# Optimization experiments

Hardware: AMD Instinct MI355X
Metric: run time of the kernel (lower is better)

Reference implementation:

```python
import jax, jax.numpy as jnp
import numpy as np

B, T, D, H = 2, 1024, 1024, 16
DH = D // H
_PAIRS = [(0, 1), (0, 2), (0, 3), (1, 2), (1, 3), (2, 3)]
_J6 = jnp.array([[0, 0, 0, 0, 0, 1],
                 [0, 0, 0, 0, -1, 0],
                 [0, 0, 0, 1, 0, 0],
                 [0, 0, 1, 0, 0, 0],
                 [0, -1, 0, 0, 0, 0],
                 [1, 0, 0, 0, 0, 0]], dtype=jnp.float32)


def exterior(p1, p2):
    # Plucker coordinates of the line through 4-vectors p1, p2, L2-normalized.
    parts = [p1[..., i] * p2[..., j] - p1[..., j] * p2[..., i] for i, j in _PAIRS]
    L = jnp.stack(parts, axis=-1)  # (..., 6)
    n = jnp.maximum(jnp.linalg.norm(L, axis=-1, keepdims=True), 1e-12)
    return L / n


def setup_inputs() -> dict:
    key = jax.random.key(0)
    ks = jax.random.split(key, 10)
    s = 0.02
    return {
        "x": jax.random.normal(ks[0], (B, T, D), jnp.float32),
        "Wqkv": jax.random.normal(ks[1], (3 * D, D), jnp.float32) * s,
        "bqkv": jnp.zeros((3 * D,), jnp.float32),
        "W1w": jax.random.normal(ks[2], (4 * H, D), jnp.float32) * s,
        "W2w": jax.random.normal(ks[3], (4 * H, D), jnp.float32) * s,
        "W1r": jax.random.normal(ks[4], (4 * H, D), jnp.float32) * s,
        "W2r": jax.random.normal(ks[5], (4 * H, D), jnp.float32) * s,
        "bias_scale": jnp.full((H,), 0.1, jnp.float32),
        "Wout": jax.random.normal(ks[6], (D, D), jnp.float32) * s,
        "bout": jnp.zeros((D,), jnp.float32),
    }


def reference(x, Wqkv, bqkv, W1w, W2w, W1r, W2r, bias_scale, Wout, bout):
    Bb, Tt, Dd = x.shape
    scale = DH ** (-0.5)
    qkv = (x @ Wqkv.T + bqkv).reshape(Bb, Tt, 3, H, DH)
    q = jnp.transpose(qkv[:, :, 0], (0, 2, 1, 3))  # (B,H,T,dh)
    k = jnp.transpose(qkv[:, :, 1], (0, 2, 1, 3))
    v = jnp.transpose(qkv[:, :, 2], (0, 2, 1, 3))
    std_logits = jnp.einsum('bhtd,bhsd->bhts', q, k) * scale

    x_prev = jnp.concatenate([jnp.zeros((Bb, 1, Dd), x.dtype), x[:, :-1]], axis=1)
    w1 = (x_prev @ W1w.T).reshape(Bb, Tt, H, 4)
    w2 = (x @ W2w.T).reshape(Bb, Tt, H, 4)
    write_lines = exterior(w1, w2)  # (B,T,H,6)
    r1 = (x @ W1r.T).reshape(Bb, Tt, H, 4)
    r2 = (x @ W2r.T).reshape(Bb, Tt, H, 4)
    read_lines = exterior(r1, r2)  # (B,T,H,6)

    Jw = jnp.einsum('bthi,ij->bhtj', write_lines, _J6)  # (B,H,T,6)
    rd = jnp.transpose(read_lines, (0, 2, 1, 3))        # (B,H,T,6)

    outer = Jw[..., :, None] * Jw[..., None, :]          # (B,H,T,6,6)
    M_causal = jnp.cumsum(outer, axis=2)                 # running Gram state
    rd_M = jnp.einsum('bhti,bhtij->bhtj', rd, M_causal)  # (B,H,T,6)
    bias_raw = jnp.einsum('bhti,bhsi->bhts', rd_M, Jw)   # (B,H,T,T)
    bias = jnp.abs(bias_raw) * bias_scale.reshape(1, H, 1, 1)

    logits = std_logits + bias
    mask = jnp.triu(jnp.ones((Tt, Tt), bool), 1)
    logits = jnp.where(mask, -jnp.inf, logits)
    attn = jax.nn.softmax(logits, axis=-1)
    out = jnp.einsum('bhts,bhsd->bthd', attn, v).reshape(Bb, Tt, Dd)
    return out @ Wout.T + bout
```

## Files before the change

kernel.cpp:

```cpp
#include <hip/hip_runtime.h>
#include <math.h>

#define B_ 2
#define T_ 1024
#define D_ 1024
#define H_ 16
#define NA_ 3328

typedef __attribute__((ext_vector_type(8))) short bf16x8;
typedef __attribute__((ext_vector_type(4))) float f32x4;

__device__ inline unsigned short f2bf(float x) {
  return (unsigned short)((__float_as_uint(x) + 0x8000u) >> 16);
}
__device__ inline unsigned bfpack(float lo, float hi) {
  unsigned a = __float_as_uint(hi) + 0x8000u;
  unsigned b = __float_as_uint(lo) + 0x8000u;
  return __builtin_amdgcn_perm(a, b, 0x07060302);
}
__device__ inline void hl_split(float x, unsigned short& h, unsigned short& l) {
  unsigned short hh = f2bf(x);
  float hf = __uint_as_float(((unsigned)hh) << 16);
  l = f2bf(x - hf);
  h = hh;
}

#define G_PRO()                                                                \
  const int tid = threadIdx.x;                                                 \
  const int w = tid >> 6, lane = tid & 63;                                     \
  const int lr = lane & 15, g = lane >> 4;                                     \
  const int wm = (w >> 1) * 64, wn = (w & 1) * 64;                             \
  const int row = tid >> 1, half = tid & 1;

#define G_LOADA(d, s) {                                                        \
  d[0] = *(const float4*)(Ap + (s) * 32);                                      \
  d[1] = *(const float4*)(Ap + (s) * 32 + 4);                                  \
  d[2] = *(const float4*)(Ap + (s) * 32 + 8);                                  \
  d[3] = *(const float4*)(Ap + (s) * 32 + 12); }
#define G_LOADB(d, s) {                                                        \
  d[0] = *(const float4*)(Bp + (s) * 32);                                      \
  d[1] = *(const float4*)(Bp + (s) * 32 + 4);                                  \
  d[2] = *(const float4*)(Bp + (s) * 32 + 8);                                  \
  d[3] = *(const float4*)(Bp + (s) * 32 + 12); }
#define G_STORE(bi, a, b) {                                                    \
  unsigned char* SA_ = Smem + (bi) * 8192;                                     \
  uint4 lo = make_uint4(bfpack(a[0].x, a[0].y), bfpack(a[0].z, a[0].w),        \
                        bfpack(a[1].x, a[1].y), bfpack(a[1].z, a[1].w));       \
  uint4 hi = make_uint4(bfpack(a[2].x, a[2].y), bfpack(a[2].z, a[2].w),        \
                        bfpack(a[3].x, a[3].y), bfpack(a[3].z, a[3].w));       \
  *(uint4*)(SA_ + (half * 2 + 0) * 2048 + row * 16) = lo;                      \
  *(uint4*)(SA_ + (half * 2 + 1) * 2048 + row * 16) = hi;                      \
  unsigned char* SB_ = Smem + 16384 + (bi) * 8192;                             \
  lo = make_uint4(bfpack(b[0].x, b[0].y), bfpack(b[0].z, b[0].w),              \
                  bfpack(b[1].x, b[1].y), bfpack(b[1].z, b[1].w));             \
  hi = make_uint4(bfpack(b[2].x, b[2].y), bfpack(b[2].z, b[2].w),              \
                  bfpack(b[3].x, b[3].y), bfpack(b[3].z, b[3].w));             \
  *(uint4*)(SB_ + (half * 2 + 0) * 2048 + row * 16) = lo;                      \
  *(uint4*)(SB_ + (half * 2 + 1) * 2048 + row * 16) = hi; }
#define G_COMPUTE(bi) {                                                        \
  const unsigned char* SA_ = Smem + (bi) * 8192;                               \
  const unsigned char* SB_ = Smem + 16384 + (bi) * 8192;                       \
  bf16x8 af[4], bfr[4];                                                        \
  _Pragma("unroll") for (int i = 0; i < 4; ++i)                                \
    af[i] = *(const bf16x8*)(SA_ + g * 2048 + (wm + i * 16 + lr) * 16);        \
  _Pragma("unroll") for (int j = 0; j < 4; ++j)                                \
    bfr[j] = *(const bf16x8*)(SB_ + g * 2048 + (wn + j * 16 + lr) * 16);       \
  _Pragma("unroll") for (int i = 0; i < 4; ++i)                                \
  _Pragma("unroll") for (int j = 0; j < 4; ++j)                                \
    acc[i][j] = __builtin_amdgcn_mfma_f32_16x16x32_bf16(af[i], bfr[j],         \
                                                        acc[i][j], 0, 0, 0); }
#define G_MAIN()                                                               \
  f32x4 acc[4][4];                                                             \
  const f32x4 zf = {0.f, 0.f, 0.f, 0.f};                                       \
  _Pragma("unroll") for (int i = 0; i < 4; ++i)                                \
  _Pragma("unroll") for (int j = 0; j < 4; ++j) acc[i][j] = zf;                \
  float4 a0[4], b0[4], a1[4], b1[4];                                           \
  G_LOADA(a0, 0); G_LOADB(b0, 0);                                              \
  G_STORE(0, a0, b0);                                                          \
  G_LOADA(a1, 1); G_LOADB(b1, 1);                                              \
  __syncthreads();                                                             \
  _Pragma("unroll 1") for (int s = 0; s < 32; s += 2) {                        \
    G_COMPUTE(0);                                                              \
    G_STORE(1, a1, b1);                                                        \
    if (s + 2 < 32) { G_LOADA(a0, s + 2); G_LOADB(b0, s + 2); }                \
    __syncthreads();                                                           \
    G_COMPUTE(1);                                                              \
    if (s + 2 < 32) G_STORE(0, a0, b0);                                        \
    if (s + 3 < 32) { G_LOADA(a1, s + 3); G_LOADB(b1, s + 3); }                \
    __syncthreads();                                                           \
  }

__global__ __launch_bounds__(256) void gemm_qkv(
    const float* __restrict__ A, const float* __restrict__ Wqkv,
    const float* __restrict__ bqkv,
    const float* __restrict__ W1w, const float* __restrict__ W2w,
    const float* __restrict__ W1r, const float* __restrict__ W2r,
    float* __restrict__ C)
{
  __shared__ __align__(16) unsigned char Smem[32768];
  const int m0 = blockIdx.y * 128, n0 = blockIdx.x * 128;
  G_PRO();
  const float* Ap = A + (size_t)(m0 + row) * 1024 + half * 16;
  const float* Bp;
  {
    const int cg = n0 + row;
    if (cg < 3072) Bp = Wqkv + (size_t)cg * 1024;
    else {
      const int r2 = cg - 3072;
      const float* Wm = (r2 < 64) ? W1w : (r2 < 128) ? W2w : (r2 < 192) ? W1r : W2r;
      Bp = Wm + (size_t)(r2 & 63) * 1024;
    }
    Bp += half * 16;
  }
  G_MAIN();
#pragma unroll
  for (int i = 0; i < 4; ++i) {
    const int rbase = m0 + wm + i * 16 + 4 * g;
#pragma unroll
    for (int j = 0; j < 4; ++j) {
      const int col = n0 + wn + j * 16 + lr;
      const float bb = (col < 3072) ? bqkv[col] : 0.f;
#pragma unroll
      for (int r = 0; r < 4; ++r)
        C[(size_t)(rbase + r) * NA_ + col] = acc[i][j][r] + bb;
    }
  }
}

__global__ __launch_bounds__(256) void gemm_out(
    const float* __restrict__ A, const float* __restrict__ Bm,
    const float* __restrict__ bias, float* __restrict__ C)
{
  __shared__ __align__(16) unsigned char Smem[32768];
  const int m0 = blockIdx.y * 128, n0 = blockIdx.x * 128;
  G_PRO();
  const float* Ap = A + (size_t)(m0 + row) * 1024 + half * 16;
  const float* Bp = Bm + (size_t)(n0 + row) * 1024 + half * 16;
  G_MAIN();
#pragma unroll
  for (int i = 0; i < 4; ++i) {
    const int rbase = m0 + wm + i * 16 + 4 * g;
#pragma unroll
    for (int j = 0; j < 4; ++j) {
      const int col = n0 + wn + j * 16 + lr;
      const float bb = bias[col];
#pragma unroll
      for (int r = 0; r < 4; ++r)
        C[(size_t)(rbase + r) * 1024 + col] = acc[i][j][r] + bb;
    }
  }
}

__global__ __launch_bounds__(256) void exterior_kernel(
    const float* __restrict__ qkvp,
    float* __restrict__ Jw, float* __restrict__ rd,
    unsigned* __restrict__ Jwpk)
{
  const int i = blockIdx.x * 256 + threadIdx.x;
  const int h = i & 15;
  const int t = (i >> 4) & 1023;
  const int b = i >> 14;
  const size_t rowt = ((size_t)(b * T_) + t) * NA_;

  float4 p1w = make_float4(0.f, 0.f, 0.f, 0.f);
  if (t > 0) p1w = *(const float4*)(qkvp + rowt - NA_ + 3072 + h * 4);
  const float4 p2w = *(const float4*)(qkvp + rowt + 3136 + h * 4);
  const float4 p1r = *(const float4*)(qkvp + rowt + 3200 + h * 4);
  const float4 p2r = *(const float4*)(qkvp + rowt + 3264 + h * 4);

  const size_t base = ((size_t)(b * H_ + h) * T_ + t) * 6;
  {
    const float L0 = p1w.x * p2w.y - p1w.y * p2w.x;
    const float L1 = p1w.x * p2w.z - p1w.z * p2w.x;
    const float L2 = p1w.x * p2w.w - p1w.w * p2w.x;
    const float L3 = p1w.y * p2w.z - p1w.z * p2w.y;
    const float L4 = p1w.y * p2w.w - p1w.w * p2w.y;
    const float L5 = p1w.z * p2w.w - p1w.w * p2w.z;
    const float n = sqrtf(L0 * L0 + L1 * L1 + L2 * L2 + L3 * L3 + L4 * L4 + L5 * L5);
    const float inv = 1.f / fmaxf(n, 1e-12f);
    float jv[6] = {L5 * inv, -L4 * inv, L3 * inv, L2 * inv, -L1 * inv, L0 * inv};
#pragma unroll
    for (int k = 0; k < 6; ++k) Jw[base + k] = jv[k];
    unsigned short JH[6], JL[6];
#pragma unroll
    for (int k = 0; k < 6; ++k) hl_split(jv[k], JH[k], JL[k]);
    unsigned* jp = Jwpk + (((size_t)(b * H_ + h) * T_ + t) << 4);
    unsigned h01 = JH[0] | ((unsigned)JH[1] << 16);
    unsigned h23 = JH[2] | ((unsigned)JH[3] << 16);
    unsigned h45 = JH[4] | ((unsigned)JH[5] << 16);
    jp[0] = h01; jp[1] = h23; jp[2] = h45;
    jp[3] = JL[0] | ((unsigned)JL[1] << 16);
    jp[4] = JL[2] | ((unsigned)JL[3] << 16);
    jp[5] = JL[4] | ((unsigned)JL[5] << 16);
    jp[6] = h01; jp[7] = h23; jp[8] = h45;
#pragma unroll
    for (int k = 9; k < 16; ++k) jp[k] = 0;
  }
  {
    const float L0 = p1r.x * p2r.y - p1r.y * p2r.x;
    const float L1 = p1r.x * p2r.z - p1r.z * p2r.x;
    const float L2 = p1r.x * p2r.w - p1r.w * p2r.x;
    const float L3 = p1r.y * p2r.z - p1r.z * p2r.y;
    const float L4 = p1r.y * p2r.w - p1r.w * p2r.y;
    const float L5 = p1r.z * p2r.w - p1r.w * p2r.z;
    const float n = sqrtf(L0 * L0 + L1 * L1 + L2 * L2 + L3 * L3 + L4 * L4 + L5 * L5);
    const float inv = 1.f / fmaxf(n, 1e-12f);
    rd[base + 0] = L0 * inv;
    rd[base + 1] = L1 * inv;
    rd[base + 2] = L2 * inv;
    rd[base + 3] = L3 * inv;
    rd[base + 4] = L4 * inv;
    rd[base + 5] = L5 * inv;
  }
}

__global__ __launch_bounds__(256) void scan_kernel(
    const float* __restrict__ Jw, const float* __restrict__ rd,
    unsigned* __restrict__ rdMpk)
{
  __shared__ float sc[256][40];
  const int tid = threadIdx.x;
  const int bh = blockIdx.x;
  const float* Jb = Jw + (size_t)bh * T_ * 6;
  const float* Rb = rd + (size_t)bh * T_ * 6;
  const int t0 = tid * 4;

  float L[36], M[36];
#pragma unroll
  for (int i = 0; i < 36; ++i) L[i] = 0.f;
  for (int tt = 0; tt < 4; ++tt) {
    float j6[6];
#pragma unroll
    for (int i = 0; i < 6; ++i) j6[i] = Jb[(size_t)(t0 + tt) * 6 + i];
#pragma unroll
    for (int a = 0; a < 6; ++a)
#pragma unroll
      for (int c = 0; c < 6; ++c)
        L[a * 6 + c] = fmaf(j6[a], j6[c], L[a * 6 + c]);
  }
#pragma unroll
  for (int i = 0; i < 36; ++i) M[i] = L[i];
#pragma unroll
  for (int k = 0; k < 9; ++k)
    *(float4*)&sc[tid][k * 4] = make_float4(M[k*4], M[k*4+1], M[k*4+2], M[k*4+3]);
  __syncthreads();

  for (int off = 1; off < 256; off <<= 1) {
    float4 tmp[9];
    const bool act = (tid >= off);
    if (act) {
#pragma unroll
      for (int k = 0; k < 9; ++k) tmp[k] = *(const float4*)&sc[tid - off][k * 4];
    }
    __syncthreads();
    if (act) {
#pragma unroll
      for (int k = 0; k < 9; ++k) {
        M[k*4]   += tmp[k].x; M[k*4+1] += tmp[k].y;
        M[k*4+2] += tmp[k].z; M[k*4+3] += tmp[k].w;
      }
#pragma unroll
      for (int k = 0; k < 9; ++k)
        *(float4*)&sc[tid][k * 4] = make_float4(M[k*4], M[k*4+1], M[k*4+2], M[k*4+3]);
    }
    __syncthreads();
  }

  float Mp[36];
#pragma unroll
  for (int i = 0; i < 36; ++i) Mp[i] = M[i] - L[i];

  for (int tt = 0; tt < 4; ++tt) {
    const int t = t0 + tt;
    float j6[6], r6[6];
#pragma unroll
    for (int i = 0; i < 6; ++i) { j6[i] = Jb[(size_t)t * 6 + i]; r6[i] = Rb[(size_t)t * 6 + i]; }
#pragma unroll
    for (int a = 0; a < 6; ++a)
#pragma unroll
      for (int c = 0; c < 6; ++c)
        Mp[a * 6 + c] = fmaf(j6[a], j6[c], Mp[a * 6 + c]);
    float s6[6];
#pragma unroll
    for (int jj = 0; jj < 6; ++jj) {
      float s = 0.f;
#pragma unroll
      for (int a = 0; a < 6; ++a) s = fmaf(r6[a], Mp[a * 6 + jj], s);
      s6[jj] = s;
    }
    unsigned short hh[6], ll[6];
#pragma unroll
    for (int i = 0; i < 6; ++i) hl_split(s6[i], hh[i], ll[i]);
    unsigned* ob = rdMpk + (((size_t)bh * T_ + t) << 4);
    unsigned h01 = hh[0] | ((unsigned)hh[1] << 16);
    unsigned h23 = hh[2] | ((unsigned)hh[3] << 16);
    unsigned h45 = hh[4] | ((unsigned)hh[5] << 16);
    ob[0] = h01; ob[1] = h23; ob[2] = h45;
    ob[3] = h01; ob[4] = h23; ob[5] = h45;
    ob[6] = ll[0] | ((unsigned)ll[1] << 16);
    ob[7] = ll[2] | ((unsigned)ll[3] << 16);
    ob[8] = ll[4] | ((unsigned)ll[5] << 16);
#pragma unroll
    for (int i = 9; i < 16; ++i) ob[i] = 0;
  }
}

__global__ __launch_bounds__(256) void attn_mfma(
    const float* __restrict__ qkvp,
    const unsigned* __restrict__ Jwpk,
    const unsigned* __restrict__ rdMpk,
    const float* __restrict__ bias_scale,
    float* __restrict__ attnout)
{
  __shared__ __align__(16) unsigned char smem[40960];
  unsigned char* KT = smem;
  unsigned char* VT = smem + 16384;
  unsigned char* PB = smem + 32768;

  const int gid = blockIdx.x;
  const int bh = gid & 31;
  const int c = (gid < 256) ? (15 - (gid >> 5)) : ((gid - 256) >> 5);
  const int b = bh >> 4, h = bh & 15;
  const int tid = threadIdx.x;
  const int w = tid >> 6;
  const int lane = tid & 63;
  const int lr = lane & 15;
  const int g = lane >> 4;
  const int t0 = c * 64;
  const int nT = c + 1;

  const float* Rows = qkvp + (size_t)b * T_ * NA_ + h * 64;
  const size_t jb = (size_t)(b * H_ + h) * T_;

  bf16x8 qa[2];
  {
    const float* qp = Rows + (size_t)(t0 + w * 16 + lr) * NA_;
#pragma unroll
    for (int kb = 0; kb < 2; ++kb) {
      const float4 f0 = *(const float4*)(qp + kb * 32 + g * 8);
      const float4 f1 = *(const float4*)(qp + kb * 32 + g * 8 + 4);
      union { uint4 u; bf16x8 v; } qq;
      qq.u = make_uint4(bfpack(f0.x, f0.y), bfpack(f0.z, f0.w),
                        bfpack(f1.x, f1.y), bfpack(f1.z, f1.w));
      qa[kb] = qq.v;
    }
  }
  bf16x8 ra = *(const bf16x8*)(rdMpk + ((jb + t0 + w * 16 + lr) << 4) + g * 4);
  const float bsc = bias_scale[h];

  float m[4], lsum[4];
  f32x4 O[4];
  const f32x4 zf = {0.f, 0.f, 0.f, 0.f};
#pragma unroll
  for (int r = 0; r < 4; ++r) { m[r] = -1e30f; lsum[r] = 0.f; }
#pragma unroll
  for (int d = 0; d < 4; ++d) O[d] = zf;

  const int kr = tid >> 2, kc = tid & 3;
  const int sp = tid & 31, d8 = tid >> 5;

  float4 kA[4], vA0, vA1, vA2, vA3, kN[4], vN0, vN1, vN2, vN3;
  {
    const float* kp = Rows + (size_t)kr * NA_ + 1024 + kc * 16;
#pragma unroll
    for (int i = 0; i < 4; ++i) kA[i] = *(const float4*)(kp + i * 4);
    const float* vr = Rows + (size_t)(2 * sp) * NA_ + 2048 + d8 * 8;
    vA0 = *(const float4*)vr;         vA1 = *(const float4*)(vr + 4);
    vA2 = *(const float4*)(vr + NA_); vA3 = *(const float4*)(vr + NA_ + 4);
  }

  for (int ti = 0; ti < nT; ++ti) {
    const int s0 = ti * 64;
    const int buf = ti & 1;
    {
      unsigned char* kt = KT + buf * 8192;
      const float e[16] = {kA[0].x, kA[0].y, kA[0].z, kA[0].w,
                           kA[1].x, kA[1].y, kA[1].z, kA[1].w,
                           kA[2].x, kA[2].y, kA[2].z, kA[2].w,
                           kA[3].x, kA[3].y, kA[3].z, kA[3].w};
      const int swz = (kr & 7) << 4;
      uint4 w0, w1;
      w0.x = bfpack(e[0], e[1]);  w0.y = bfpack(e[2], e[3]);
      w0.z = bfpack(e[4], e[5]);  w0.w = bfpack(e[6], e[7]);
      w1.x = bfpack(e[8], e[9]);  w1.y = bfpack(e[10], e[11]);
      w1.z = bfpack(e[12], e[13]); w1.w = bfpack(e[14], e[15]);
      *(uint4*)(kt + kr * 128 + ((kc * 32) ^ swz))      = w0;
      *(uint4*)(kt + kr * 128 + ((kc * 32 + 16) ^ swz)) = w1;
    }
    {
      unsigned* vt = (unsigned*)(VT + buf * 8192);
      const float r0[8] = {vA0.x, vA0.y, vA0.z, vA0.w, vA1.x, vA1.y, vA1.z, vA1.w};
      const float r1[8] = {vA2.x, vA2.y, vA2.z, vA2.w, vA3.x, vA3.y, vA3.z, vA3.w};
#pragma unroll
      for (int i = 0; i < 8; ++i) {
        const int d = d8 * 8 + i;
        vt[d * 32 + (sp ^ ((d & 7) << 2))] = bfpack(r0[i], r1[i]);
      }
    }
    if (ti + 1 < nT) {
      const float* kp = Rows + (size_t)(s0 + 64 + kr) * NA_ + 1024 + kc * 16;
#pragma unroll
      for (int i = 0; i < 4; ++i) kN[i] = *(const float4*)(kp + i * 4);
      const float* vr = Rows + (size_t)(s0 + 64 + 2 * sp) * NA_ + 2048 + d8 * 8;
      vN0 = *(const float4*)vr;         vN1 = *(const float4*)(vr + 4);
      vN2 = *(const float4*)(vr + NA_); vN3 = *(const float4*)(vr + NA_ + 4);
    }
    __syncthreads();

    f32x4 S[4], Sb[4];
    const unsigned char* kt = KT + buf * 8192;
    __builtin_amdgcn_s_setprio(1);
#pragma unroll
    for (int cb = 0; cb < 4; ++cb) {
      const int srw = cb * 16 + lr;
      f32x4 a = zf;
#pragma unroll
      for (int kb = 0; kb < 2; ++kb) {
        const bf16x8 kf = *(const bf16x8*)(kt + srw * 128 + (((kb * 64) + 16 * g) ^ ((srw & 7) << 4)));
        a = __builtin_amdgcn_mfma_f32_16x16x32_bf16(qa[kb], kf, a, 0, 0, 0);
      }
      S[cb] = a;
      const bf16x8 jw = *(const bf16x8*)(Jwpk + ((jb + s0 + cb * 16 + lr) << 4) + g * 4);
      Sb[cb] = __builtin_amdgcn_mfma_f32_16x16x32_bf16(ra, jw, zf, 0, 0, 0);
    }
    __builtin_amdgcn_s_setprio(0);

    const bool diag = (s0 == t0);
    float logit[4][4];
#pragma unroll
    for (int cb = 0; cb < 4; ++cb) {
#pragma unroll
      for (int r = 0; r < 4; ++r) {
        float lg = S[cb][r] * 0.125f + fabsf(Sb[cb][r]) * bsc;
        if (diag && (cb * 16 + lr > w * 16 + 4 * g + r)) lg = -1e30f;
        logit[cb][r] = lg;
      }
    }
#pragma unroll
    for (int r = 0; r < 4; ++r) {
      float mx = fmaxf(fmaxf(logit[0][r], logit[1][r]), fmaxf(logit[2][r], logit[3][r]));
      mx = fmaxf(mx, __shfl_xor(mx, 1));
      mx = fmaxf(mx, __shfl_xor(mx, 2));
      mx = fmaxf(mx, __shfl_xor(mx, 4));
      mx = fmaxf(mx, __shfl_xor(mx, 8));
      const float nm = fmaxf(m[r], mx);
      const float sc = __expf(m[r] - nm);
      m[r] = nm;
      lsum[r] *= sc;
#pragma unroll
      for (int d = 0; d < 4; ++d) O[d][r] *= sc;
    }
#pragma unroll
    for (int cb = 0; cb < 4; ++cb) {
#pragma unroll
      for (int r = 0; r < 4; ++r) {
        const float p = __expf(logit[cb][r] - m[r]);
        lsum[r] += p;
        const int q = 4 * g + r;
        const int s = cb * 16 + lr;
        const int byte = w * 2048 + q * 128 + ((2 * s) ^ ((q & 7) << 4));
        *(unsigned short*)(PB + byte) = f2bf(p);
      }
    }
    asm volatile("s_waitcnt lgkmcnt(0)" ::: "memory");
    __builtin_amdgcn_sched_barrier(0);

    bf16x8 pa[2];
#pragma unroll
    for (int kb = 0; kb < 2; ++kb) {
      const int byte = w * 2048 + lr * 128 + (((kb * 64) + 16 * g) ^ ((lr & 7) << 4));
      pa[kb] = *(const bf16x8*)(PB + byte);
    }
    const unsigned char* vtb = VT + buf * 8192;
    __builtin_amdgcn_s_setprio(1);
#pragma unroll
    for (int db = 0; db < 4; ++db) {
      const int d = db * 16 + lr;
#pragma unroll
      for (int kb = 0; kb < 2; ++kb) {
        const int byte = d * 128 + (((kb * 64) + 16 * g) ^ ((d & 7) << 4));
        const bf16x8 vf = *(const bf16x8*)(vtb + byte);
        O[db] = __builtin_amdgcn_mfma_f32_16x16x32_bf16(pa[kb], vf, O[db], 0, 0, 0);
      }
    }
    __builtin_amdgcn_s_setprio(0);
#pragma unroll
    for (int i = 0; i < 4; ++i) kA[i] = kN[i];
    vA0 = vN0; vA1 = vN1; vA2 = vN2; vA3 = vN3;
  }

#pragma unroll
  for (int r = 0; r < 4; ++r) {
    float l = lsum[r];
    l += __shfl_xor(l, 1);
    l += __shfl_xor(l, 2);
    l += __shfl_xor(l, 4);
    l += __shfl_xor(l, 8);
    lsum[r] = 1.f / l;
  }
  {
    const int qb = w * 16 + 4 * g;
#pragma unroll
    for (int db = 0; db < 4; ++db) {
#pragma unroll
      for (int r = 0; r < 4; ++r) {
        const int t = t0 + qb + r;
        attnout[(size_t)(b * T_ + t) * 1024 + h * 64 + db * 16 + lr] = O[db][r] * lsum[r];
      }
    }
  }
}

extern "C" void kernel_launch(void* const* d_in, const int* in_sizes, int n_in,
                              void* d_out, int out_size, void* d_ws, size_t ws_size,
                              hipStream_t stream)
{
  (void)in_sizes; (void)n_in; (void)out_size; (void)ws_size;
  const float* x    = (const float*)d_in[0];
  const float* Wqkv = (const float*)d_in[1];
  const float* bqkv = (const float*)d_in[2];
  const float* W1w  = (const float*)d_in[3];
  const float* W2w  = (const float*)d_in[4];
  const float* W1r  = (const float*)d_in[5];
  const float* W2r  = (const float*)d_in[6];
  const float* bsc  = (const float*)d_in[7];
  const float* Wout = (const float*)d_in[8];
  const float* bout = (const float*)d_in[9];
  float* out = (float*)d_out;

  float*    qkvp    = (float*)d_ws;
  float*    Jw      = qkvp + (size_t)2048 * NA_;
  float*    rd      = Jw + 196608;
  unsigned* Jwpk    = (unsigned*)(rd + 196608);
  unsigned* rdMpk   = Jwpk + 524288;
  float*    attnout = (float*)(rdMpk + 524288);

  gemm_qkv<<<dim3(26, 16), 256, 0, stream>>>(
      x, Wqkv, bqkv, W1w, W2w, W1r, W2r, qkvp);
  exterior_kernel<<<dim3(B_ * T_ * H_ / 256), 256, 0, stream>>>(
      qkvp, Jw, rd, Jwpk);
  scan_kernel<<<dim3(B_ * H_), 256, 0, stream>>>(Jw, rd, rdMpk);
  attn_mfma<<<dim3(B_ * H_ * (T_ / 64)), 256, 0, stream>>>(
      qkvp, Jwpk, rdMpk, bsc, attnout);
  gemm_out<<<dim3(8, 16), 256, 0, stream>>>(attnout, Wout, bout, out);
}
```

Baseline: 128.9 us.

## Fuse exterior into scan kernel and add lazy softmax max rescaling

Merges the Plucker exterior computation into the scan kernel, which now recomputes write and read lines from the qkv projection directly. This removes one launch and the fp32 Jw/rd intermediate buffers. The cost is that all of it runs in only 32 blocks, with each thread redoing the write-line math twice. Separately, attention skips the online-softmax rescale of O and lsum unless some row max grows by more than 8, using a wave-wide any. This saves exp and multiplies but lets the exponent values grow, which is safe only within that bound.

```diff
diff --git a/kernel.cpp b/kernel.cpp
--- a/kernel.cpp
+++ b/kernel.cpp
@@ -151,25 +151,26 @@
   }
 }
 
-__global__ __launch_bounds__(256) void exterior_kernel(
+__global__ __launch_bounds__(256) void scan_kernel(
     const float* __restrict__ qkvp,
-    float* __restrict__ Jw, float* __restrict__ rd,
-    unsigned* __restrict__ Jwpk)
+    unsigned* __restrict__ Jwpk, unsigned* __restrict__ rdMpk)
 {
-  const int i = blockIdx.x * 256 + threadIdx.x;
-  const int h = i & 15;
-  const int t = (i >> 4) & 1023;
-  const int b = i >> 14;
-  const size_t rowt = ((size_t)(b * T_) + t) * NA_;
-
-  float4 p1w = make_float4(0.f, 0.f, 0.f, 0.f);
-  if (t > 0) p1w = *(const float4*)(qkvp + rowt - NA_ + 3072 + h * 4);
-  const float4 p2w = *(const float4*)(qkvp + rowt + 3136 + h * 4);
-  const float4 p1r = *(const float4*)(qkvp + rowt + 3200 + h * 4);
-  const float4 p2r = *(const float4*)(qkvp + rowt + 3264 + h * 4);
-
-  const size_t base = ((size_t)(b * H_ + h) * T_ + t) * 6;
-  {
+  __shared__ float sc[256][41];
+  const int tid = threadIdx.x;
+  const int bh = blockIdx.x;
+  const int b = bh >> 4, h = bh & 15;
+  const int t0 = tid * 4;
+
+  float L[36];
+#pragma unroll
+  for (int i = 0; i < 36; ++i) L[i] = 0.f;
+
+  for (int tt = 0; tt < 4; ++tt) {
+    const int t = t0 + tt;
+    const size_t rowt = ((size_t)(b * T_) + t) * NA_;
+    float4 p1w = make_float4(0.f, 0.f, 0.f, 0.f);
+    if (t > 0) p1w = *(const float4*)(qkvp + rowt - NA_ + 3072 + h * 4);
+    const float4 p2w = *(const float4*)(qkvp + rowt + 3136 + h * 4);
     const float L0 = p1w.x * p2w.y - p1w.y * p2w.x;
     const float L1 = p1w.x * p2w.z - p1w.z * p2w.x;
     const float L2 = p1w.x * p2w.w - p1w.w * p2w.x;
@@ -178,16 +179,14 @@
     const float L5 = p1w.z * p2w.w - p1w.w * p2w.z;
     const float n = sqrtf(L0 * L0 + L1 * L1 + L2 * L2 + L3 * L3 + L4 * L4 + L5 * L5);
     const float inv = 1.f / fmaxf(n, 1e-12f);
-    float jv[6] = {L5 * inv, -L4 * inv, L3 * inv, L2 * inv, -L1 * inv, L0 * inv};
-#pragma unroll
-    for (int k = 0; k < 6; ++k) Jw[base + k] = jv[k];
+    const float jv[6] = {L5 * inv, -L4 * inv, L3 * inv, L2 * inv, -L1 * inv, L0 * inv};
     unsigned short JH[6], JL[6];
 #pragma unroll
     for (int k = 0; k < 6; ++k) hl_split(jv[k], JH[k], JL[k]);
-    unsigned* jp = Jwpk + (((size_t)(b * H_ + h) * T_ + t) << 4);
-    unsigned h01 = JH[0] | ((unsigned)JH[1] << 16);
-    unsigned h23 = JH[2] | ((unsigned)JH[3] << 16);
-    unsigned h45 = JH[4] | ((unsigned)JH[5] << 16);
+    unsigned* jp = Jwpk + (((size_t)bh * T_ + t) << 4);
+    const unsigned h01 = JH[0] | ((unsigned)JH[1] << 16);
+    const unsigned h23 = JH[2] | ((unsigned)JH[3] << 16);
+    const unsigned h45 = JH[4] | ((unsigned)JH[5] << 16);
     jp[0] = h01; jp[1] = h23; jp[2] = h45;
     jp[3] = JL[0] | ((unsigned)JL[1] << 16);
     jp[4] = JL[2] | ((unsigned)JL[3] << 16);
@@ -195,56 +194,20 @@
     jp[6] = h01; jp[7] = h23; jp[8] = h45;
 #pragma unroll
     for (int k = 9; k < 16; ++k) jp[k] = 0;
-  }
-  {
-    const float L0 = p1r.x * p2r.y - p1r.y * p2r.x;
-    const float L1 = p1r.x * p2r.z - p1r.z * p2r.x;
-    const float L2 = p1r.x * p2r.w - p1r.w * p2r.x;
-    const float L3 = p1r.y * p2r.z - p1r.z * p2r.y;
-    const float L4 = p1r.y * p2r.w - p1r.w * p2r.y;
-    const float L5 = p1r.z * p2r.w - p1r.w * p2r.z;
-    const float n = sqrtf(L0 * L0 + L1 * L1 + L2 * L2 + L3 * L3 + L4 * L4 + L5 * L5);
-    const float inv = 1.f / fmaxf(n, 1e-12f);
-    rd[base + 0] = L0 * inv;
-    rd[base + 1] = L1 * inv;
-    rd[base + 2] = L2 * inv;
-    rd[base + 3] = L3 * inv;
-    rd[base + 4] = L4 * inv;
-    rd[base + 5] = L5 * inv;
-  }
-}
-
-__global__ __launch_bounds__(256) void scan_kernel(
-    const float* __restrict__ Jw, const float* __restrict__ rd,
-    unsigned* __restrict__ rdMpk)
-{
-  __shared__ float sc[256][40];
-  const int tid = threadIdx.x;
-  const int bh = blockIdx.x;
-  const float* Jb = Jw + (size_t)bh * T_ * 6;
-  const float* Rb = rd + (size_t)bh * T_ * 6;
-  const int t0 = tid * 4;
-
-  float L[36], M[36];
-#pragma unroll
-  for (int i = 0; i < 36; ++i) L[i] = 0.f;
-  for (int tt = 0; tt < 4; ++tt) {
-    float j6[6];
-#pragma unroll
-    for (int i = 0; i < 6; ++i) j6[i] = Jb[(size_t)(t0 + tt) * 6 + i];
 #pragma unroll
     for (int a = 0; a < 6; ++a)
 #pragma unroll
-      for (int c = 0; c < 6; ++c)
-        L[a * 6 + c] = fmaf(j6[a], j6[c], L[a * 6 + c]);
-  }
+      for (int c2 = 0; c2 < 6; ++c2)
+        L[a * 6 + c2] = fmaf(jv[a], jv[c2], L[a * 6 + c2]);
+  }
+
+  float M[36];
 #pragma unroll
   for (int i = 0; i < 36; ++i) M[i] = L[i];
 #pragma unroll
   for (int k = 0; k < 9; ++k)
     *(float4*)&sc[tid][k * 4] = make_float4(M[k*4], M[k*4+1], M[k*4+2], M[k*4+3]);
   __syncthreads();
-
   for (int off = 1; off < 256; off <<= 1) {
     float4 tmp[9];
     const bool act = (tid >= off);
@@ -272,29 +235,57 @@
 
   for (int tt = 0; tt < 4; ++tt) {
     const int t = t0 + tt;
-    float j6[6], r6[6];
-#pragma unroll
-    for (int i = 0; i < 6; ++i) { j6[i] = Jb[(size_t)t * 6 + i]; r6[i] = Rb[(size_t)t * 6 + i]; }
+    const size_t rowt = ((size_t)(b * T_) + t) * NA_;
+    float4 p1w = make_float4(0.f, 0.f, 0.f, 0.f);
+    if (t > 0) p1w = *(const float4*)(qkvp + rowt - NA_ + 3072 + h * 4);
+    const float4 p2w = *(const float4*)(qkvp + rowt + 3136 + h * 4);
+    const float4 p1r = *(const float4*)(qkvp + rowt + 3200 + h * 4);
+    const float4 p2r = *(const float4*)(qkvp + rowt + 3264 + h * 4);
+    float jv[6], rv[6];
+    {
+      const float L0 = p1w.x * p2w.y - p1w.y * p2w.x;
+      const float L1 = p1w.x * p2w.z - p1w.z * p2w.x;
+      const float L2 = p1w.x * p2w.w - p1w.w * p2w.x;
+      const float L3 = p1w.y * p2w.z - p1w.z * p2w.y;
+      const float L4 = p1w.y * p2w.w - p1w.w * p2w.y;
+      const float L5 = p1w.z * p2w.w - p1w.w * p2w.z;
+      const float n = sqrtf(L0*L0 + L1*L1 + L2*L2 + L3*L3 + L4*L4 + L5*L5);
+      const float inv = 1.f / fmaxf(n, 1e-12f);
+      jv[0] = L5*inv; jv[1] = -L4*inv; jv[2] = L3*inv;
+      jv[3] = L2*inv; jv[4] = -L1*inv; jv[5] = L0*inv;
+    }
+    {
+      const float L0 = p1r.x * p2r.y - p1r.y * p2r.x;
+      const float L1 = p1r.x * p2r.z - p1r.z * p2r.x;
+      const float L2 = p1r.x * p2r.w - p1r.w * p2r.x;
+      const float L3 = p1r.y * p2r.z - p1r.z * p2r.y;
+      const float L4 = p1r.y * p2r.w - p1r.w * p2r.y;
+      const float L5 = p1r.z * p2r.w - p1r.w * p2r.z;
+      const float n = sqrtf(L0*L0 + L1*L1 + L2*L2 + L3*L3 + L4*L4 + L5*L5);
+      const float inv = 1.f / fmaxf(n, 1e-12f);
+      rv[0] = L0*inv; rv[1] = L1*inv; rv[2] = L2*inv;
+      rv[3] = L3*inv; rv[4] = L4*inv; rv[5] = L5*inv;
+    }
 #pragma unroll
     for (int a = 0; a < 6; ++a)
 #pragma unroll
-      for (int c = 0; c < 6; ++c)
-        Mp[a * 6 + c] = fmaf(j6[a], j6[c], Mp[a * 6 + c]);
+      for (int c2 = 0; c2 < 6; ++c2)
+        Mp[a * 6 + c2] = fmaf(jv[a], jv[c2], Mp[a * 6 + c2]);
     float s6[6];
 #pragma unroll
     for (int jj = 0; jj < 6; ++jj) {
       float s = 0.f;
 #pragma unroll
-      for (int a = 0; a < 6; ++a) s = fmaf(r6[a], Mp[a * 6 + jj], s);
+      for (int a = 0; a < 6; ++a) s = fmaf(rv[a], Mp[a * 6 + jj], s);
       s6[jj] = s;
     }
     unsigned short hh[6], ll[6];
 #pragma unroll
     for (int i = 0; i < 6; ++i) hl_split(s6[i], hh[i], ll[i]);
     unsigned* ob = rdMpk + (((size_t)bh * T_ + t) << 4);
-    unsigned h01 = hh[0] | ((unsigned)hh[1] << 16);
-    unsigned h23 = hh[2] | ((unsigned)hh[3] << 16);
-    unsigned h45 = hh[4] | ((unsigned)hh[5] << 16);
+    const unsigned h01 = hh[0] | ((unsigned)hh[1] << 16);
+    const unsigned h23 = hh[2] | ((unsigned)hh[3] << 16);
+    const unsigned h45 = hh[4] | ((unsigned)hh[5] << 16);
     ob[0] = h01; ob[1] = h23; ob[2] = h45;
     ob[3] = h01; ob[4] = h23; ob[5] = h45;
     ob[6] = ll[0] | ((unsigned)ll[1] << 16);
@@ -436,6 +427,7 @@
         logit[cb][r] = lg;
       }
     }
+    float mxr[4];
 #pragma unroll
     for (int r = 0; r < 4; ++r) {
       float mx = fmaxf(fmaxf(logit[0][r], logit[1][r]), fmaxf(logit[2][r], logit[3][r]));
@@ -443,12 +435,21 @@
       mx = fmaxf(mx, __shfl_xor(mx, 2));
       mx = fmaxf(mx, __shfl_xor(mx, 4));
       mx = fmaxf(mx, __shfl_xor(mx, 8));
-      const float nm = fmaxf(m[r], mx);
-      const float sc = __expf(m[r] - nm);
-      m[r] = nm;
-      lsum[r] *= sc;
-#pragma unroll
-      for (int d = 0; d < 4; ++d) O[d][r] *= sc;
+      mxr[r] = mx;
+    }
+    bool need = false;
+#pragma unroll
+    for (int r = 0; r < 4; ++r) need = need || (mxr[r] > m[r] + 8.f);
+    if (__any(need)) {
+#pragma unroll
+      for (int r = 0; r < 4; ++r) {
+        const float nm = fmaxf(m[r], mxr[r]);
+        const float sc = __expf(m[r] - nm);
+        m[r] = nm;
+        lsum[r] *= sc;
+#pragma unroll
+        for (int d = 0; d < 4; ++d) O[d][r] *= sc;
+      }
     }
 #pragma unroll
     for (int cb = 0; cb < 4; ++cb) {
@@ -529,17 +530,13 @@
   float* out = (float*)d_out;
 
   float*    qkvp    = (float*)d_ws;
-  float*    Jw      = qkvp + (size_t)2048 * NA_;
-  float*    rd      = Jw + 196608;
-  unsigned* Jwpk    = (unsigned*)(rd + 196608);
+  unsigned* Jwpk    = (unsigned*)(qkvp + (size_t)2048 * NA_);
   unsigned* rdMpk   = Jwpk + 524288;
   float*    attnout = (float*)(rdMpk + 524288);
 
   gemm_qkv<<<dim3(26, 16), 256, 0, stream>>>(
       x, Wqkv, bqkv, W1w, W2w, W1r, W2r, qkvp);
-  exterior_kernel<<<dim3(B_ * T_ * H_ / 256), 256, 0, stream>>>(
-      qkvp, Jw, rd, Jwpk);
-  scan_kernel<<<dim3(B_ * H_), 256, 0, stream>>>(Jw, rd, rdMpk);
+  scan_kernel<<<dim3(B_ * H_), 256, 0, stream>>>(qkvp, Jwpk, rdMpk);
   attn_mfma<<<dim3(B_ * H_ * (T_ / 64)), 256, 0, stream>>>(
       qkvp, Jwpk, rdMpk, bsc, attnout);
   gemm_out<<<dim3(8, 16), 256, 0, stream>>>(attnout, Wout, bout, out);
```

Result: slower. 133.9 us (+3.9%).
